# Performance work log

Hardware: AMD Instinct MI355X
Metric: run time of the kernel (lower is better)

## Reference

```python
import jax, jax.numpy as jnp
import numpy as np

V_ENC, V_DEC = 30000, 30000
E_ENC, E_DEC = 256, 256
H = 512
B, S = 64, 48


def gru_cell(x, h, w_ih, w_hh, b_ih, b_hh):
    # torch GRUCell math. x: [B,E], h: [B,H], w_ih: [3H,E], w_hh: [3H,H]
    gi = x @ w_ih.T + b_ih
    gh = h @ w_hh.T + b_hh
    i_r, i_z, i_n = jnp.split(gi, 3, axis=-1)
    h_r, h_z, h_n = jnp.split(gh, 3, axis=-1)
    r = jax.nn.sigmoid(i_r + h_r)
    z = jax.nn.sigmoid(i_z + h_z)
    n = jnp.tanh(i_n + r * h_n)
    return (1.0 - z) * n + z * h


def setup_inputs() -> dict:
    key = jax.random.key(0)
    ks = jax.random.split(key, 14)
    p = lambda k, shp: jax.random.normal(k, shp, dtype=jnp.float32) * 0.05
    return {
        "input_tensor": jax.random.randint(ks[0], (B, S), 0, V_ENC),
        "enc_embed": p(ks[1], (V_ENC, E_ENC)),
        "enc_wih": p(ks[2], (3 * H, E_ENC)),
        "enc_whh": p(ks[3], (3 * H, H)),
        "enc_bih": p(ks[4], (3 * H,)),
        "enc_bhh": p(ks[5], (3 * H,)),
        "dec_embed": p(ks[6], (V_DEC, E_DEC)),
        "dec_wih": p(ks[7], (3 * H, E_DEC)),
        "dec_whh": p(ks[8], (3 * H, H)),
        "dec_bih": p(ks[9], (3 * H,)),
        "dec_bhh": p(ks[10], (3 * H,)),
        "proj_w": p(ks[11], (V_DEC, 2 * H)),
        "proj_b": p(ks[12], (V_DEC,)),
    }


def reference(input_tensor, enc_embed, enc_wih, enc_whh, enc_bih, enc_bhh,
              dec_embed, dec_wih, dec_whh, dec_bih, dec_bhh, proj_w, proj_b):
    batch = input_tensor.shape[0]
    # --- encoder: embedding + GRU over sequence ---
    x_seq = enc_embed[input_tensor]                       # [B,S,E]
    x_seq = jnp.swapaxes(x_seq, 0, 1)                     # [S,B,E]
    h0 = jnp.zeros((batch, H), dtype=enc_embed.dtype)

    def enc_step(h, x):
        h_new = gru_cell(x, h, enc_wih, enc_whh, enc_bih, enc_bhh)
        return h_new, h_new

    enc_last, enc_states = jax.lax.scan(enc_step, h0, x_seq)
    enc_states = jnp.swapaxes(enc_states, 0, 1)           # [B,S,H]

    dec_input0 = jnp.zeros((batch,), dtype=jnp.int32)

    def dec_step(carry, _):
        h, tok = carry
        x = dec_embed[tok]                                # [B,E]
        h_new = gru_cell(x, h, dec_wih, dec_whh, dec_bih, dec_bhh)
        # dot-product attention: decoder hidden vs encoder states
        scores = jnp.einsum("bsh,bh->bs", enc_states, h_new)
        attn = jax.nn.softmax(scores, axis=-1)
        context = jnp.einsum("bs,bsh->bh", attn, enc_states)
        cat = jnp.concatenate([h_new, context], axis=-1)  # [B,2H]
        logits = cat @ proj_w.T + proj_b                  # [B,V]
        log_probs = jax.nn.log_softmax(logits, axis=-1)
        topi = jnp.argmax(log_probs, axis=-1).astype(jnp.int32)
        return (h_new, topi), (topi, log_probs)

    _, (predicted, dists) = jax.lax.scan(
        dec_step, (enc_last, dec_input0), None, length=input_tensor.shape[1])
    return predicted, dists  # [S,B] int, [S,B,V] log-probs
```

## Files before the change

kernel.cpp:

```cpp
#include <hip/hip_runtime.h>
#include <math.h>

#define BB 64
#define SS 48
#define EE 256
#define HH 512
#define VV 30000
#define G3 1536
#define NPB 235
#define TAU 0.04f

typedef __attribute__((ext_vector_type(8))) short s8v;
typedef __attribute__((ext_vector_type(4))) short s4v;
typedef __attribute__((ext_vector_type(4))) float f4v;

__device__ __forceinline__ float sigmoidf_(float x) { return 1.f / (1.f + expf(-x)); }

__device__ __forceinline__ short f2bf(float x) {
    union { float f; unsigned u; } v; v.f = x;
    unsigned r = v.u + 0x7fffu + ((v.u >> 16) & 1u);
    return (short)(r >> 16);
}

__global__ __launch_bounds__(256) void split_hi_kernel(
    const float* __restrict__ src, long n4, short* __restrict__ hi)
{
    for (long i = (long)blockIdx.x * 256 + threadIdx.x; i < n4;
         i += (long)gridDim.x * 256) {
        const float4 x = *(const float4*)&src[i * 4];
        s4v h;
        h[0] = f2bf(x.x); h[1] = f2bf(x.y); h[2] = f2bf(x.z); h[3] = f2bf(x.w);
        *(s4v*)&hi[i * 4] = h;
    }
}

__global__ __launch_bounds__(256) void enc_gi_all_kernel(
    const int* __restrict__ input,
    const float* __restrict__ embed,
    const float* __restrict__ wih,
    float* __restrict__ gi_all)
{
    __shared__ float Wt[64][68];
    __shared__ float Xt[64][68];
    const int t  = threadIdx.x;
    const int tx = t & 15, ty = t >> 4;
    const int j0 = blockIdx.x * 64;
    const int s  = blockIdx.y;
    const int bb = t & 63, kq = t >> 6;
    const int wkk = (t & 15) * 4, wjj = t >> 4;

    const long xrow = (long)input[bb * SS + s] * EE;
    float* gi = gi_all + (long)s * G3 * BB;

    float acc[4][4];
    #pragma unroll
    for (int i = 0; i < 4; i++)
        #pragma unroll
        for (int j = 0; j < 4; j++) acc[i][j] = 0.f;

    for (int kb = 0; kb < EE; kb += 64) {
        #pragma unroll
        for (int r = 0; r < 4; r++) {
            int row = j0 + wjj + r * 16;
            const float4 w = *(const float4*)&wih[row * EE + kb + wkk];
            Wt[wkk + 0][wjj + r * 16] = w.x;
            Wt[wkk + 1][wjj + r * 16] = w.y;
            Wt[wkk + 2][wjj + r * 16] = w.z;
            Wt[wkk + 3][wjj + r * 16] = w.w;
        }
        {
            const float* src = embed + xrow + kb + kq * 16;
            #pragma unroll
            for (int q = 0; q < 4; q++) {
                const float4 x = *(const float4*)&src[q * 4];
                Xt[kq * 16 + q * 4 + 0][bb] = x.x;
                Xt[kq * 16 + q * 4 + 1][bb] = x.y;
                Xt[kq * 16 + q * 4 + 2][bb] = x.z;
                Xt[kq * 16 + q * 4 + 3][bb] = x.w;
            }
        }
        __syncthreads();
        #pragma unroll 8
        for (int k = 0; k < 64; k++) {
            const float4 a = *(const float4*)&Wt[k][ty * 4];
            const float4 x = *(const float4*)&Xt[k][tx * 4];
            acc[0][0] += a.x * x.x; acc[0][1] += a.x * x.y; acc[0][2] += a.x * x.z; acc[0][3] += a.x * x.w;
            acc[1][0] += a.y * x.x; acc[1][1] += a.y * x.y; acc[1][2] += a.y * x.z; acc[1][3] += a.y * x.w;
            acc[2][0] += a.z * x.x; acc[2][1] += a.z * x.y; acc[2][2] += a.z * x.z; acc[2][3] += a.z * x.w;
            acc[3][0] += a.w * x.x; acc[3][1] += a.w * x.y; acc[3][2] += a.w * x.z; acc[3][3] += a.w * x.w;
        }
        __syncthreads();
    }
    #pragma unroll
    for (int i = 0; i < 4; i++) {
        float4 o; o.x = acc[i][0]; o.y = acc[i][1]; o.z = acc[i][2]; o.w = acc[i][3];
        *(float4*)&gi[(j0 + ty * 4 + i) * BB + tx * 4] = o;
    }
}

__global__ __launch_bounds__(256) void enc_step_kernel(
    const float* __restrict__ gi_s,
    const float* __restrict__ whh,
    const float* __restrict__ bih, const float* __restrict__ bhh,
    const float* __restrict__ hprev,
    int s,
    float* __restrict__ enc_states)
{
    __shared__ __attribute__((aligned(16))) float Wt[64][52];
    __shared__ __attribute__((aligned(16))) float Xt[64][68];
    const int t = threadIdx.x;
    const int tx = t & 15, ty = t >> 4;
    const int bb = t & 63, kq = t >> 6;
    const int wlr = t >> 4, wc4 = (t & 15) * 4;
    const int h0 = blockIdx.x * 16;

    float accr[4] = {0.f, 0.f, 0.f, 0.f};
    float accz[4] = {0.f, 0.f, 0.f, 0.f};
    float acchn[4] = {0.f, 0.f, 0.f, 0.f};

    if (hprev) {
        const float* xr = hprev + (long)bb * (SS * HH);
        for (int kb = 0; kb < HH; kb += 64) {
            #pragma unroll
            for (int g = 0; g < 3; g++) {
                const float4 w = *(const float4*)&whh[(long)(g * HH + h0 + wlr) * HH + kb + wc4];
                Wt[wc4 + 0][g * 16 + wlr] = w.x;
                Wt[wc4 + 1][g * 16 + wlr] = w.y;
                Wt[wc4 + 2][g * 16 + wlr] = w.z;
                Wt[wc4 + 3][g * 16 + wlr] = w.w;
            }
            {
                const float* src = xr + kb + kq * 16;
                #pragma unroll
                for (int q = 0; q < 4; q++) {
                    const float4 x = *(const float4*)&src[q * 4];
                    Xt[kq * 16 + q * 4 + 0][bb] = x.x;
                    Xt[kq * 16 + q * 4 + 1][bb] = x.y;
                    Xt[kq * 16 + q * 4 + 2][bb] = x.z;
                    Xt[kq * 16 + q * 4 + 3][bb] = x.w;
                }
            }
            __syncthreads();
            #pragma unroll 4
            for (int k = 0; k < 64; k++) {
                float wr = Wt[k][ty], wz = Wt[k][16 + ty], wn = Wt[k][32 + ty];
                const float4 x = *(const float4*)&Xt[k][tx * 4];
                accr[0] += wr * x.x; accr[1] += wr * x.y; accr[2] += wr * x.z; accr[3] += wr * x.w;
                accz[0] += wz * x.x; accz[1] += wz * x.y; accz[2] += wz * x.z; accz[3] += wz * x.w;
                acchn[0] += wn * x.x; acchn[1] += wn * x.y; acchn[2] += wn * x.z; acchn[3] += wn * x.w;
            }
            __syncthreads();
        }
    }

    const int j = h0 + ty;
    const float br = bih[j] + bhh[j];
    const float bz = bih[HH + j] + bhh[HH + j];
    const float bin = bih[2 * HH + j];
    const float bhn = bhh[2 * HH + j];
    const float4 gr4 = *(const float4*)&gi_s[(long)j * BB + tx * 4];
    const float4 gz4 = *(const float4*)&gi_s[(long)(HH + j) * BB + tx * 4];
    const float4 gn4 = *(const float4*)&gi_s[(long)(2 * HH + j) * BB + tx * 4];
    const float grs[4] = {gr4.x, gr4.y, gr4.z, gr4.w};
    const float gzs[4] = {gz4.x, gz4.y, gz4.z, gz4.w};
    const float gns[4] = {gn4.x, gn4.y, gn4.z, gn4.w};
    #pragma unroll
    for (int i = 0; i < 4; i++) {
        int b = tx * 4 + i;
        float r = sigmoidf_(grs[i] + accr[i] + br);
        float z = sigmoidf_(gzs[i] + accz[i] + bz);
        float n = tanhf(gns[i] + bin + r * (acchn[i] + bhn));
        float hp = hprev ? hprev[(long)b * (SS * HH) + j] : 0.f;
        enc_states[((long)b * SS + s) * HH + j] = (1.f - z) * n + z * hp;
    }
}

__global__ __launch_bounds__(256) void dec_step_kernel(
    const int* __restrict__ tok, int s,
    const float* __restrict__ embed,
    const float* __restrict__ wih, const float* __restrict__ whh,
    const float* __restrict__ bih, const float* __restrict__ bhh,
    const float* __restrict__ hprev, long hstride,
    float* __restrict__ hbuf)
{
    __shared__ __attribute__((aligned(16))) float Wt[64][52];
    __shared__ __attribute__((aligned(16))) float Xt[64][68];
    const int t = threadIdx.x;
    const int tx = t & 15, ty = t >> 4;
    const int bb = t & 63, kq = t >> 6;
    const int wlr = t >> 4, wc4 = (t & 15) * 4;
    const int h0 = blockIdx.x * 16;

    float accr[4] = {0.f, 0.f, 0.f, 0.f};
    float accz[4] = {0.f, 0.f, 0.f, 0.f};
    float accin[4] = {0.f, 0.f, 0.f, 0.f};
    float acchn[4] = {0.f, 0.f, 0.f, 0.f};

    {
        const int tk = (s == 0) ? 0 : tok[bb];
        const float* xr = embed + (long)tk * EE;
        for (int kb = 0; kb < EE; kb += 64) {
            #pragma unroll
            for (int g = 0; g < 3; g++) {
                const float4 w = *(const float4*)&wih[(long)(g * HH + h0 + wlr) * EE + kb + wc4];
                Wt[wc4 + 0][g * 16 + wlr] = w.x;
                Wt[wc4 + 1][g * 16 + wlr] = w.y;
                Wt[wc4 + 2][g * 16 + wlr] = w.z;
                Wt[wc4 + 3][g * 16 + wlr] = w.w;
            }
            {
                const float* src = xr + kb + kq * 16;
                #pragma unroll
                for (int q = 0; q < 4; q++) {
                    const float4 x = *(const float4*)&src[q * 4];
                    Xt[kq * 16 + q * 4 + 0][bb] = x.x;
                    Xt[kq * 16 + q * 4 + 1][bb] = x.y;
                    Xt[kq * 16 + q * 4 + 2][bb] = x.z;
                    Xt[kq * 16 + q * 4 + 3][bb] = x.w;
                }
            }
            __syncthreads();
            #pragma unroll 4
            for (int k = 0; k < 64; k++) {
                float wr = Wt[k][ty], wz = Wt[k][16 + ty], wn = Wt[k][32 + ty];
                const float4 x = *(const float4*)&Xt[k][tx * 4];
                accr[0] += wr * x.x; accr[1] += wr * x.y; accr[2] += wr * x.z; accr[3] += wr * x.w;
                accz[0] += wz * x.x; accz[1] += wz * x.y; accz[2] += wz * x.z; accz[3] += wz * x.w;
                accin[0] += wn * x.x; accin[1] += wn * x.y; accin[2] += wn * x.z; accin[3] += wn * x.w;
            }
            __syncthreads();
        }
    }
    {
        const float* xr = hprev + (long)bb * hstride;
        for (int kb = 0; kb < HH; kb += 64) {
            #pragma unroll
            for (int g = 0; g < 3; g++) {
                const float4 w = *(const float4*)&whh[(long)(g * HH + h0 + wlr) * HH + kb + wc4];
                Wt[wc4 + 0][g * 16 + wlr] = w.x;
                Wt[wc4 + 1][g * 16 + wlr] = w.y;
                Wt[wc4 + 2][g * 16 + wlr] = w.z;
                Wt[wc4 + 3][g * 16 + wlr] = w.w;
            }
            {
                const float* src = xr + kb + kq * 16;
                #pragma unroll
                for (int q = 0; q < 4; q++) {
                    const float4 x = *(const float4*)&src[q * 4];
                    Xt[kq * 16 + q * 4 + 0][bb] = x.x;
                    Xt[kq * 16 + q * 4 + 1][bb] = x.y;
                    Xt[kq * 16 + q * 4 + 2][bb] = x.z;
                    Xt[kq * 16 + q * 4 + 3][bb] = x.w;
                }
            }
            __syncthreads();
            #pragma unroll 4
            for (int k = 0; k < 64; k++) {
                float wr = Wt[k][ty], wz = Wt[k][16 + ty], wn = Wt[k][32 + ty];
                const float4 x = *(const float4*)&Xt[k][tx * 4];
                accr[0] += wr * x.x; accr[1] += wr * x.y; accr[2] += wr * x.z; accr[3] += wr * x.w;
                accz[0] += wz * x.x; accz[1] += wz * x.y; accz[2] += wz * x.z; accz[3] += wz * x.w;
                acchn[0] += wn * x.x; acchn[1] += wn * x.y; acchn[2] += wn * x.z; acchn[3] += wn * x.w;
            }
            __syncthreads();
        }
    }

    const int j = h0 + ty;
    const float br = bih[j] + bhh[j];
    const float bz = bih[HH + j] + bhh[HH + j];
    const float bin = bih[2 * HH + j];
    const float bhn = bhh[2 * HH + j];
    #pragma unroll
    for (int i = 0; i < 4; i++) {
        int b = tx * 4 + i;
        float r = sigmoidf_(accr[i] + br);
        float z = sigmoidf_(accz[i] + bz);
        float n = tanhf(accin[i] + bin + r * (acchn[i] + bhn));
        float hp = hprev[(long)b * hstride + j];
        hbuf[b * HH + j] = (1.f - z) * n + z * hp;
    }
}

__global__ __launch_bounds__(256) void dec_attn_kernel(
    const float* __restrict__ hbuf,
    const float* __restrict__ enc_states,
    float* __restrict__ cat_f32,
    short* __restrict__ cat_hi)
{
    int b = blockIdx.x, t = threadIdx.x;
    __shared__ float hs[HH];
    __shared__ float ctxs[HH];
    __shared__ float sc[SS];

    for (int j = t; j < HH; j += 256) hs[j] = hbuf[b * HH + j];
    __syncthreads();

    int wave = t >> 6, lane = t & 63;
    for (int sp = wave; sp < SS; sp += 4) {
        const float* es = enc_states + ((long)b * SS + sp) * HH;
        float p = 0.f;
        for (int k = lane; k < HH; k += 64) p += es[k] * hs[k];
        for (int o = 32; o; o >>= 1) p += __shfl_down(p, o);
        if (lane == 0) sc[sp] = p;
    }
    __syncthreads();
    if (t == 0) {
        float m = sc[0];
        for (int i = 1; i < SS; i++) m = fmaxf(m, sc[i]);
        float sum = 0.f;
        for (int i = 0; i < SS; i++) { float e = expf(sc[i] - m); sc[i] = e; sum += e; }
        float inv = 1.f / sum;
        for (int i = 0; i < SS; i++) sc[i] *= inv;
    }
    __syncthreads();
    for (int j = t; j < HH; j += 256) {
        float c = 0.f;
        for (int sp = 0; sp < SS; sp++) c += sc[sp] * enc_states[((long)b * SS + sp) * HH + j];
        ctxs[j] = c;
    }
    __syncthreads();
    for (int k = t; k < 2 * HH; k += 256) {
        float val = (k < HH) ? hs[k] : ctxs[k - HH];
        cat_f32[b * 2 * HH + k] = val;
        cat_hi[b * 2 * HH + k] = f2bf(val);
    }
}

__global__ __launch_bounds__(256) void proj_hi_kernel(
    const short* __restrict__ pw_hi,
    const float* __restrict__ pw_f32,
    const short* __restrict__ cat_hi,
    const float* __restrict__ pb,
    float* __restrict__ logits,
    float* __restrict__ pm, float* __restrict__ ps)
{
    __shared__ __attribute__((aligned(16))) char smem_raw[64 * 129 * 4];
    short (*Ah)[72] = (short(*)[72])smem_raw;
    short (*Bh)[72] = (short(*)[72])(smem_raw + 128 * 72 * 2);
    float (*LT)[129] = (float(*)[129])smem_raw;
    __shared__ float sm4[4][64];
    __shared__ float ss4[4][64];

    const int t = threadIdx.x;
    const int lane = t & 63, wave = t >> 6;
    const int v0 = blockIdx.x * 128;

    f4v acc[2][4];
    #pragma unroll
    for (int i = 0; i < 2; i++)
        #pragma unroll
        for (int j = 0; j < 4; j++) acc[i][j] = (f4v){0.f, 0.f, 0.f, 0.f};

    for (int ks = 0; ks < 16; ks++) {
        const int kb = ks * 64;
        if (pw_hi) {
            #pragma unroll
            for (int p = 0; p < 4; p++) {
                int idx = p * 256 + t;
                int r = idx >> 3, c8 = (idx & 7) * 8;
                long vrow = v0 + r; if (vrow >= VV) vrow = VV - 1;
                *(s8v*)&Ah[r][c8] = *(const s8v*)&pw_hi[vrow * 1024 + kb + c8];
            }
        } else {
            #pragma unroll
            for (int p = 0; p < 4; p++) {
                int idx = p * 256 + t;
                int r = idx >> 3, c8 = (idx & 7) * 8;
                long vrow = v0 + r; if (vrow >= VV) vrow = VV - 1;
                const float* src = &pw_f32[vrow * 1024 + kb + c8];
                const float4 f0 = *(const float4*)&src[0];
                const float4 f1 = *(const float4*)&src[4];
                s8v h;
                h[0] = f2bf(f0.x); h[1] = f2bf(f0.y); h[2] = f2bf(f0.z); h[3] = f2bf(f0.w);
                h[4] = f2bf(f1.x); h[5] = f2bf(f1.y); h[6] = f2bf(f1.z); h[7] = f2bf(f1.w);
                *(s8v*)&Ah[r][c8] = h;
            }
        }
        #pragma unroll
        for (int p = 0; p < 2; p++) {
            int idx = p * 256 + t;
            int r = idx >> 3, c8 = (idx & 7) * 8;
            *(s8v*)&Bh[r][c8] = *(const s8v*)&cat_hi[r * 1024 + kb + c8];
        }
        __syncthreads();
        #pragma unroll
        for (int kc = 0; kc < 64; kc += 32) {
            const int ko = kc + (lane >> 4) * 8;
            const int fr = lane & 15;
            s8v ah0 = *(s8v*)&Ah[wave * 32 + fr][ko];
            s8v ah1 = *(s8v*)&Ah[wave * 32 + 16 + fr][ko];
            s8v bh[4];
            #pragma unroll
            for (int fb = 0; fb < 4; fb++) bh[fb] = *(s8v*)&Bh[fb * 16 + fr][ko];
            #pragma unroll
            for (int fb = 0; fb < 4; fb++) {
                acc[0][fb] = __builtin_amdgcn_mfma_f32_16x16x32_bf16(ah0, bh[fb], acc[0][fb], 0, 0, 0);
                acc[1][fb] = __builtin_amdgcn_mfma_f32_16x16x32_bf16(ah1, bh[fb], acc[1][fb], 0, 0, 0);
            }
        }
        __syncthreads();
    }

    const int col = lane & 15;
    #pragma unroll
    for (int fv = 0; fv < 2; fv++) {
        int rloc = wave * 32 + fv * 16 + (lane >> 4) * 4;
        int vbase = v0 + rloc;
        float pbv[4];
        #pragma unroll
        for (int i = 0; i < 4; i++) pbv[i] = (vbase + i < VV) ? pb[vbase + i] : 0.f;
        #pragma unroll
        for (int fb = 0; fb < 4; fb++) {
            int b = fb * 16 + col;
            float o[4];
            #pragma unroll
            for (int i = 0; i < 4; i++) o[i] = acc[fv][fb][i] + pbv[i];
            if (vbase + 3 < VV) {
                float4 st; st.x = o[0]; st.y = o[1]; st.z = o[2]; st.w = o[3];
                *(float4*)&logits[(long)b * VV + vbase] = st;
            } else {
                for (int i = 0; i < 4; i++)
                    if (vbase + i < VV) logits[(long)b * VV + vbase + i] = o[i];
            }
            #pragma unroll
            for (int i = 0; i < 4; i++)
                LT[b][rloc + i] = (vbase + i < VV) ? o[i] : -INFINITY;
        }
    }
    __syncthreads();

    {
        int b = t & 63, q = t >> 6;
        float m = -INFINITY, s = 0.f;
        for (int r = q * 32; r < q * 32 + 32; r++) {
            float v = LT[b][r];
            if (v == -INFINITY) continue;
            if (v > m) { s = s * expf(m - v) + 1.f; m = v; }
            else s += expf(v - m);
        }
        sm4[q][b] = m; ss4[q][b] = s;
    }
    __syncthreads();
    if (t < 64) {
        int b = t;
        float M = sm4[0][b], S = ss4[0][b];
        #pragma unroll
        for (int q = 1; q < 4; q++) {
            float m2 = sm4[q][b], s2 = ss4[q][b];
            if (m2 > M) { S = S * expf(M - m2) + s2; M = m2; }
            else if (m2 != -INFINITY) S += s2 * expf(m2 - M);
        }
        pm[blockIdx.x * 64 + b] = M;
        ps[blockIdx.x * 64 + b] = S;
    }
}

__global__ __launch_bounds__(256) void reduce_par_kernel(
    const float* __restrict__ logits,
    const float* __restrict__ pm, const float* __restrict__ ps,
    const float* __restrict__ pw_f32, const float* __restrict__ pb,
    const float* __restrict__ cat_f32,
    int* __restrict__ tok, float* __restrict__ pred_out, float* __restrict__ lse_out)
{
    int b = blockIdx.x, t = threadIdx.x;
    int lane = t & 63, wave = t >> 6;
    __shared__ float red[256], red2[256];
    __shared__ float cf[2 * HH];
    __shared__ int   qlist[32];
    __shared__ int   vlist[32];
    __shared__ float ws4[4];
    __shared__ float bestv;
    __shared__ int   besti, qcnt, vcnt;

    for (int k = t; k < 2 * HH; k += 256) cf[k] = cat_f32[b * 2 * HH + k];
    if (t == 0) { qcnt = 0; vcnt = 0; bestv = -INFINITY; besti = 0; }

    float pmv = -INFINITY, psv = 0.f;
    if (t < NPB) { pmv = pm[t * 64 + b]; psv = ps[t * 64 + b]; }
    red[t] = pmv; red2[t] = psv;
    __syncthreads();
    for (int o = 128; o; o >>= 1) {
        if (t < o) {
            float m1 = red[t],     s1 = red2[t];
            float m2 = red[t + o], s2 = red2[t + o];
            if (m2 > m1) { red[t] = m2; red2[t] = s2 + s1 * expf(m1 - m2); }
            else if (m2 != -INFINITY) red2[t] = s1 + s2 * expf(m2 - m1);
        }
        __syncthreads();
    }
    float gm  = red[0];
    float lse = gm + logf(red2[0]);
    float thr = gm - TAU;

    if (t < NPB && pmv >= thr) {
        int p = atomicAdd(&qcnt, 1);
        if (p < 32) qlist[p] = t;
    }
    __syncthreads();
    int qn = qcnt; if (qn > 32) qn = 32;

    for (int qi = 0; qi < qn; qi++) {
        int ib = qlist[qi];
        if (t < 128) {
            int v = ib * 128 + t;
            if (v < VV) {
                float lv = logits[(long)b * VV + v];
                if (lv >= thr) {
                    int p = atomicAdd(&vcnt, 1);
                    if (p < 32) vlist[p] = v;
                }
            }
        }
    }
    __syncthreads();
    int nv = vcnt; if (nv > 32) nv = 32;

    for (int c = 0; c < nv; c++) {
        int vr = vlist[c];
        float p = 0.f;
        for (int k = t; k < 2 * HH; k += 256)
            p += pw_f32[(long)vr * 2 * HH + k] * cf[k];
        for (int o = 32; o; o >>= 1) p += __shfl_down(p, o);
        if (lane == 0) ws4[wave] = p;
        __syncthreads();
        if (t == 0) {
            float val = ws4[0] + ws4[1] + ws4[2] + ws4[3] + pb[vr];
            if (val > bestv || (val == bestv && vr < besti)) { bestv = val; besti = vr; }
        }
        __syncthreads();
    }
    if (t == 0) {
        tok[b] = besti;
        pred_out[b] = (float)besti;
        lse_out[b] = lse;
    }
}

__global__ void normalize_kernel(float* __restrict__ dists, const float* __restrict__ stats) {
    const long total4 = (long)SS * BB * VV / 4;
    for (long i4 = (long)blockIdx.x * blockDim.x + threadIdx.x; i4 < total4;
         i4 += (long)gridDim.x * blockDim.x) {
        long i = i4 * 4;
        int sb = (int)(i / VV);
        float st = stats[sb];
        float4 x = *(float4*)&dists[i];
        x.x -= st; x.y -= st; x.z -= st; x.w -= st;
        *(float4*)&dists[i] = x;
    }
}

extern "C" void kernel_launch(void* const* d_in, const int* in_sizes, int n_in,
                              void* d_out, int out_size, void* d_ws, size_t ws_size,
                              hipStream_t stream) {
    const int*   input     = (const int*)  d_in[0];
    const float* enc_embed = (const float*)d_in[1];
    const float* enc_wih   = (const float*)d_in[2];
    const float* enc_whh   = (const float*)d_in[3];
    const float* enc_bih   = (const float*)d_in[4];
    const float* enc_bhh   = (const float*)d_in[5];
    const float* dec_embed = (const float*)d_in[6];
    const float* dec_wih   = (const float*)d_in[7];
    const float* dec_whh   = (const float*)d_in[8];
    const float* dec_bih   = (const float*)d_in[9];
    const float* dec_bhh   = (const float*)d_in[10];
    const float* proj_w    = (const float*)d_in[11];
    const float* proj_b    = (const float*)d_in[12];

    float* out       = (float*)d_out;
    float* pred_out  = out;
    float* dists_out = out + SS * BB;

    float* ws = (float*)d_ws;
    long off = 0;
    float* enc_states = ws + off; off += (long)BB * SS * HH;
    float* gi_all     = ws + off; off += (long)SS * G3 * BB;
    float* hbuf       = ws + off; off += BB * HH;
    float* cat_f32    = ws + off; off += BB * 2 * HH;
    short* cat_hi     = (short*)(ws + off); off += BB * 2 * HH / 2;
    float* pm         = ws + off; off += NPB * 64;
    float* ps         = ws + off; off += NPB * 64;
    float* lse_arr    = ws + off; off += SS * BB;
    int*   tok        = (int*)(ws + off); off += BB;

    const long pw_elems = (long)VV * 2 * HH;
    bool use_split = ((long)ws_size >= (off + pw_elems / 2) * 4 + 1024);
    short* pw_hi = nullptr;
    if (use_split) {
        pw_hi = (short*)(ws + off);
        split_hi_kernel<<<2048, 256, 0, stream>>>(proj_w, pw_elems / 4, pw_hi);
    }

    enc_gi_all_kernel<<<dim3(G3 / 64, SS), 256, 0, stream>>>(input, enc_embed, enc_wih, gi_all);
    for (int s = 0; s < SS; s++) {
        const float* hprev = s ? enc_states + (long)(s - 1) * HH : nullptr;
        enc_step_kernel<<<HH / 16, 256, 0, stream>>>(
            gi_all + (long)s * G3 * BB, enc_whh, enc_bih, enc_bhh,
            hprev, s, enc_states);
    }

    for (int s = 0; s < SS; s++) {
        const float* hprev; long hstride;
        if (s == 0) { hprev = enc_states + (long)(SS - 1) * HH; hstride = (long)SS * HH; }
        else        { hprev = cat_f32;                          hstride = 2 * HH; }

        dec_step_kernel<<<HH / 16, 256, 0, stream>>>(tok, s, dec_embed,
                                                     dec_wih, dec_whh, dec_bih, dec_bhh,
                                                     hprev, hstride, hbuf);
        dec_attn_kernel<<<BB, 256, 0, stream>>>(hbuf, enc_states, cat_f32, cat_hi);
        float* logits = dists_out + (long)s * BB * VV;
        proj_hi_kernel<<<NPB, 256, 0, stream>>>(pw_hi, proj_w, cat_hi, proj_b, logits, pm, ps);
        reduce_par_kernel<<<BB, 256, 0, stream>>>(logits, pm, ps, proj_w, proj_b, cat_f32,
                                                  tok, pred_out + s * BB, lse_arr + s * BB);
    }

    normalize_kernel<<<2048, 256, 0, stream>>>(dists_out, lse_arr);
}
```

Measured before the change: 6.169 ms.

## Persist encoder recurrence in one kernel and fuse decoder GRU, attention, argmax

```diff
diff --git a/kernel.cpp b/kernel.cpp
--- a/kernel.cpp
+++ b/kernel.cpp
@@ -20,6 +20,9 @@
     union { float f; unsigned u; } v; v.f = x;
     unsigned r = v.u + 0x7fffu + ((v.u >> 16) & 1u);
     return (short)(r >> 16);
+}
+__device__ __forceinline__ float dot4_(float4 a, float4 b) {
+    return a.x * b.x + a.y * b.y + a.z * b.z + a.w * b.w;
 }
 
 __global__ __launch_bounds__(256) void split_hi_kernel(
@@ -98,205 +101,195 @@
     }
 }
 
-__global__ __launch_bounds__(256) void enc_step_kernel(
-    const float* __restrict__ gi_s,
+__global__ __launch_bounds__(256) void enc_all_kernel(
+    const float* __restrict__ gi_all,
     const float* __restrict__ whh,
     const float* __restrict__ bih, const float* __restrict__ bhh,
-    const float* __restrict__ hprev,
-    int s,
     float* __restrict__ enc_states)
 {
-    __shared__ __attribute__((aligned(16))) float Wt[64][52];
-    __shared__ __attribute__((aligned(16))) float Xt[64][68];
-    const int t = threadIdx.x;
-    const int tx = t & 15, ty = t >> 4;
-    const int bb = t & 63, kq = t >> 6;
-    const int wlr = t >> 4, wc4 = (t & 15) * 4;
-    const int h0 = blockIdx.x * 16;
-
-    float accr[4] = {0.f, 0.f, 0.f, 0.f};
-    float accz[4] = {0.f, 0.f, 0.f, 0.f};
-    float acchn[4] = {0.f, 0.f, 0.f, 0.f};
-
-    if (hprev) {
-        const float* xr = hprev + (long)bb * (SS * HH);
-        for (int kb = 0; kb < HH; kb += 64) {
-            #pragma unroll
-            for (int g = 0; g < 3; g++) {
-                const float4 w = *(const float4*)&whh[(long)(g * HH + h0 + wlr) * HH + kb + wc4];
-                Wt[wc4 + 0][g * 16 + wlr] = w.x;
-                Wt[wc4 + 1][g * 16 + wlr] = w.y;
-                Wt[wc4 + 2][g * 16 + wlr] = w.z;
-                Wt[wc4 + 3][g * 16 + wlr] = w.w;
-            }
-            {
-                const float* src = xr + kb + kq * 16;
-                #pragma unroll
-                for (int q = 0; q < 4; q++) {
-                    const float4 x = *(const float4*)&src[q * 4];
-                    Xt[kq * 16 + q * 4 + 0][bb] = x.x;
-                    Xt[kq * 16 + q * 4 + 1][bb] = x.y;
-                    Xt[kq * 16 + q * 4 + 2][bb] = x.z;
-                    Xt[kq * 16 + q * 4 + 3][bb] = x.w;
-                }
-            }
-            __syncthreads();
-            #pragma unroll 4
-            for (int k = 0; k < 64; k++) {
-                float wr = Wt[k][ty], wz = Wt[k][16 + ty], wn = Wt[k][32 + ty];
-                const float4 x = *(const float4*)&Xt[k][tx * 4];
-                accr[0] += wr * x.x; accr[1] += wr * x.y; accr[2] += wr * x.z; accr[3] += wr * x.w;
-                accz[0] += wz * x.x; accz[1] += wz * x.y; accz[2] += wz * x.z; accz[3] += wz * x.w;
-                acchn[0] += wn * x.x; acchn[1] += wn * x.y; acchn[2] += wn * x.z; acchn[3] += wn * x.w;
-            }
-            __syncthreads();
-        }
-    }
-
-    const int j = h0 + ty;
-    const float br = bih[j] + bhh[j];
-    const float bz = bih[HH + j] + bhh[HH + j];
-    const float bin = bih[2 * HH + j];
-    const float bhn = bhh[2 * HH + j];
-    const float4 gr4 = *(const float4*)&gi_s[(long)j * BB + tx * 4];
-    const float4 gz4 = *(const float4*)&gi_s[(long)(HH + j) * BB + tx * 4];
-    const float4 gn4 = *(const float4*)&gi_s[(long)(2 * HH + j) * BB + tx * 4];
-    const float grs[4] = {gr4.x, gr4.y, gr4.z, gr4.w};
-    const float gzs[4] = {gz4.x, gz4.y, gz4.z, gz4.w};
-    const float gns[4] = {gn4.x, gn4.y, gn4.z, gn4.w};
-    #pragma unroll
-    for (int i = 0; i < 4; i++) {
-        int b = tx * 4 + i;
-        float r = sigmoidf_(grs[i] + accr[i] + br);
-        float z = sigmoidf_(gzs[i] + accz[i] + bz);
-        float n = tanhf(gns[i] + bin + r * (acchn[i] + bhn));
-        float hp = hprev ? hprev[(long)b * (SS * HH) + j] : 0.f;
-        enc_states[((long)b * SS + s) * HH + j] = (1.f - z) * n + z * hp;
-    }
-}
-
-__global__ __launch_bounds__(256) void dec_step_kernel(
-    const int* __restrict__ tok, int s,
+    const int b = blockIdx.x, t = threadIdx.x;
+    const int lane = t & 63, wave = t >> 6;
+    __shared__ float hp[2][HH];
+
+    for (int j = t; j < HH; j += 256) {
+        float gr = gi_all[(long)j * BB + b];
+        float gz = gi_all[(long)(HH + j) * BB + b];
+        float gn = gi_all[(long)(2 * HH + j) * BB + b];
+        float r = sigmoidf_(gr + bih[j] + bhh[j]);
+        float z = sigmoidf_(gz + bih[HH + j] + bhh[HH + j]);
+        float n = tanhf(gn + bih[2 * HH + j] + r * bhh[2 * HH + j]);
+        float h = (1.f - z) * n;
+        hp[0][j] = h;
+        enc_states[((long)b * SS) * HH + j] = h;
+    }
+    __syncthreads();
+
+    for (int s = 1; s < SS; s++) {
+        const int cur = (s - 1) & 1, nxt = s & 1;
+        const float* gis = gi_all + (long)s * G3 * BB;
+        const float4 x0 = *(const float4*)&hp[cur][lane * 8];
+        const float4 x1 = *(const float4*)&hp[cur][lane * 8 + 4];
+        for (int i = 0; i < 128; i++) {
+            const int j = wave * 128 + i;
+            const float* wr = whh + (long)j * HH + lane * 8;
+            const float* wz = whh + (long)(HH + j) * HH + lane * 8;
+            const float* wn = whh + (long)(2 * HH + j) * HH + lane * 8;
+            float pr = dot4_(*(const float4*)&wr[0], x0) + dot4_(*(const float4*)&wr[4], x1);
+            float pz = dot4_(*(const float4*)&wz[0], x0) + dot4_(*(const float4*)&wz[4], x1);
+            float pn = dot4_(*(const float4*)&wn[0], x0) + dot4_(*(const float4*)&wn[4], x1);
+            #pragma unroll
+            for (int o = 32; o; o >>= 1) {
+                pr += __shfl_down(pr, o);
+                pz += __shfl_down(pz, o);
+                pn += __shfl_down(pn, o);
+            }
+            if (lane == 0) {
+                float gr = gis[(long)j * BB + b];
+                float gz = gis[(long)(HH + j) * BB + b];
+                float gn = gis[(long)(2 * HH + j) * BB + b];
+                float r = sigmoidf_(gr + pr + bih[j] + bhh[j]);
+                float z = sigmoidf_(gz + pz + bih[HH + j] + bhh[HH + j]);
+                float n = tanhf(gn + bih[2 * HH + j] + r * (pn + bhh[2 * HH + j]));
+                float h = (1.f - z) * n + z * hp[cur][j];
+                hp[nxt][j] = h;
+                enc_states[((long)b * SS + s) * HH + j] = h;
+            }
+        }
+        __syncthreads();
+    }
+}
+
+__global__ __launch_bounds__(256) void dec_fused_kernel(
+    int s,
+    const float* __restrict__ pm, const float* __restrict__ ps,
+    const float* __restrict__ logits_prev,
+    const float* __restrict__ pw_f32, const float* __restrict__ pb,
+    float* __restrict__ pred_out, float* __restrict__ lse_arr,
     const float* __restrict__ embed,
     const float* __restrict__ wih, const float* __restrict__ whh,
     const float* __restrict__ bih, const float* __restrict__ bhh,
-    const float* __restrict__ hprev, long hstride,
-    float* __restrict__ hbuf)
+    const float* __restrict__ enc_states,
+    float* __restrict__ cat_f32, short* __restrict__ cat_hi)
 {
-    __shared__ __attribute__((aligned(16))) float Wt[64][52];
-    __shared__ __attribute__((aligned(16))) float Xt[64][68];
-    const int t = threadIdx.x;
-    const int tx = t & 15, ty = t >> 4;
-    const int bb = t & 63, kq = t >> 6;
-    const int wlr = t >> 4, wc4 = (t & 15) * 4;
-    const int h0 = blockIdx.x * 16;
-
-    float accr[4] = {0.f, 0.f, 0.f, 0.f};
-    float accz[4] = {0.f, 0.f, 0.f, 0.f};
-    float accin[4] = {0.f, 0.f, 0.f, 0.f};
-    float acchn[4] = {0.f, 0.f, 0.f, 0.f};
+    const int b = blockIdx.x, t = threadIdx.x;
+    const int lane = t & 63, wave = t >> 6;
+    __shared__ float cf[2 * HH];
+    __shared__ float xe[EE];
+    __shared__ float hs[HH], ctxs[HH], sc[SS];
+    __shared__ float red[256], red2[256];
+    __shared__ int qlist[32], vlist[32];
+    __shared__ float ws4[4];
+    __shared__ float bestv;
+    __shared__ int besti, qcnt, vcnt;
+
+    int tk = 0;
+
+    if (s > 0) {
+        for (int k = t; k < 2 * HH; k += 256) cf[k] = cat_f32[(long)b * 2 * HH + k];
+        if (t == 0) { qcnt = 0; vcnt = 0; bestv = -INFINITY; besti = 0; }
+
+        float pmv = -INFINITY, psv = 0.f;
+        if (t < NPB) { pmv = pm[t * 64 + b]; psv = ps[t * 64 + b]; }
+        red[t] = pmv; red2[t] = psv;
+        __syncthreads();
+        for (int o = 128; o; o >>= 1) {
+            if (t < o) {
+                float m1 = red[t],     s1 = red2[t];
+                float m2 = red[t + o], s2 = red2[t + o];
+                if (m2 > m1) { red[t] = m2; red2[t] = s2 + s1 * expf(m1 - m2); }
+                else if (m2 != -INFINITY) red2[t] = s1 + s2 * expf(m2 - m1);
+            }
+            __syncthreads();
+        }
+        float gm  = red[0];
+        float lse = gm + logf(red2[0]);
+        float thr = gm - TAU;
+
+        if (t < NPB && pmv >= thr) {
+            int p = atomicAdd(&qcnt, 1);
+            if (p < 32) qlist[p] = t;
+        }
+        __syncthreads();
+        int qn = qcnt; if (qn > 32) qn = 32;
+        for (int qi = 0; qi < qn; qi++) {
+            int ib = qlist[qi];
+            if (t < 128) {
+                int v = ib * 128 + t;
+                if (v < VV) {
+                    float lv = logits_prev[(long)b * VV + v];
+                    if (lv >= thr) {
+                        int p = atomicAdd(&vcnt, 1);
+                        if (p < 32) vlist[p] = v;
+                    }
+                }
+            }
+        }
+        __syncthreads();
+        int nv = vcnt; if (nv > 32) nv = 32;
+        for (int c = 0; c < nv; c++) {
+            int vr = vlist[c];
+            float p = 0.f;
+            for (int k = t; k < 2 * HH; k += 256)
+                p += pw_f32[(long)vr * 2 * HH + k] * cf[k];
+            for (int o = 32; o; o >>= 1) p += __shfl_down(p, o);
+            if (lane == 0) ws4[wave] = p;
+            __syncthreads();
+            if (t == 0) {
+                float val = ws4[0] + ws4[1] + ws4[2] + ws4[3] + pb[vr];
+                if (val > bestv || (val == bestv && vr < besti)) { bestv = val; besti = vr; }
+            }
+            __syncthreads();
+        }
+        if (t == 0) {
+            pred_out[(s - 1) * BB + b] = (float)besti;
+            lse_arr[(s - 1) * BB + b] = lse;
+        }
+        __syncthreads();
+        tk = besti;
+    } else {
+        for (int j = t; j < HH; j += 256)
+            cf[j] = enc_states[((long)b * SS + (SS - 1)) * HH + j];
+        __syncthreads();
+    }
+
+    for (int k = t; k < EE; k += 256) xe[k] = embed[(long)tk * EE + k];
+    __syncthreads();
 
     {
-        const int tk = (s == 0) ? 0 : tok[bb];
-        const float* xr = embed + (long)tk * EE;
-        for (int kb = 0; kb < EE; kb += 64) {
-            #pragma unroll
-            for (int g = 0; g < 3; g++) {
-                const float4 w = *(const float4*)&wih[(long)(g * HH + h0 + wlr) * EE + kb + wc4];
-                Wt[wc4 + 0][g * 16 + wlr] = w.x;
-                Wt[wc4 + 1][g * 16 + wlr] = w.y;
-                Wt[wc4 + 2][g * 16 + wlr] = w.z;
-                Wt[wc4 + 3][g * 16 + wlr] = w.w;
-            }
-            {
-                const float* src = xr + kb + kq * 16;
-                #pragma unroll
-                for (int q = 0; q < 4; q++) {
-                    const float4 x = *(const float4*)&src[q * 4];
-                    Xt[kq * 16 + q * 4 + 0][bb] = x.x;
-                    Xt[kq * 16 + q * 4 + 1][bb] = x.y;
-                    Xt[kq * 16 + q * 4 + 2][bb] = x.z;
-                    Xt[kq * 16 + q * 4 + 3][bb] = x.w;
-                }
-            }
-            __syncthreads();
-            #pragma unroll 4
-            for (int k = 0; k < 64; k++) {
-                float wr = Wt[k][ty], wz = Wt[k][16 + ty], wn = Wt[k][32 + ty];
-                const float4 x = *(const float4*)&Xt[k][tx * 4];
-                accr[0] += wr * x.x; accr[1] += wr * x.y; accr[2] += wr * x.z; accr[3] += wr * x.w;
-                accz[0] += wz * x.x; accz[1] += wz * x.y; accz[2] += wz * x.z; accz[3] += wz * x.w;
-                accin[0] += wn * x.x; accin[1] += wn * x.y; accin[2] += wn * x.z; accin[3] += wn * x.w;
-            }
-            __syncthreads();
-        }
-    }
-    {
-        const float* xr = hprev + (long)bb * hstride;
-        for (int kb = 0; kb < HH; kb += 64) {
-            #pragma unroll
-            for (int g = 0; g < 3; g++) {
-                const float4 w = *(const float4*)&whh[(long)(g * HH + h0 + wlr) * HH + kb + wc4];
-                Wt[wc4 + 0][g * 16 + wlr] = w.x;
-                Wt[wc4 + 1][g * 16 + wlr] = w.y;
-                Wt[wc4 + 2][g * 16 + wlr] = w.z;
-                Wt[wc4 + 3][g * 16 + wlr] = w.w;
-            }
-            {
-                const float* src = xr + kb + kq * 16;
-                #pragma unroll
-                for (int q = 0; q < 4; q++) {
-                    const float4 x = *(const float4*)&src[q * 4];
-                    Xt[kq * 16 + q * 4 + 0][bb] = x.x;
-                    Xt[kq * 16 + q * 4 + 1][bb] = x.y;
-                    Xt[kq * 16 + q * 4 + 2][bb] = x.z;
-                    Xt[kq * 16 + q * 4 + 3][bb] = x.w;
-                }
-            }
-            __syncthreads();
-            #pragma unroll 4
-            for (int k = 0; k < 64; k++) {
-                float wr = Wt[k][ty], wz = Wt[k][16 + ty], wn = Wt[k][32 + ty];
-                const float4 x = *(const float4*)&Xt[k][tx * 4];
-                accr[0] += wr * x.x; accr[1] += wr * x.y; accr[2] += wr * x.z; accr[3] += wr * x.w;
-                accz[0] += wz * x.x; accz[1] += wz * x.y; accz[2] += wz * x.z; accz[3] += wz * x.w;
-                acchn[0] += wn * x.x; acchn[1] += wn * x.y; acchn[2] += wn * x.z; acchn[3] += wn * x.w;
-            }
-            __syncthreads();
-        }
-    }
-
-    const int j = h0 + ty;
-    const float br = bih[j] + bhh[j];
-    const float bz = bih[HH + j] + bhh[HH + j];
-    const float bin = bih[2 * HH + j];
-    const float bhn = bhh[2 * HH + j];
-    #pragma unroll
-    for (int i = 0; i < 4; i++) {
-        int b = tx * 4 + i;
-        float r = sigmoidf_(accr[i] + br);
-        float z = sigmoidf_(accz[i] + bz);
-        float n = tanhf(accin[i] + bin + r * (acchn[i] + bhn));
-        float hp = hprev[(long)b * hstride + j];
-        hbuf[b * HH + j] = (1.f - z) * n + z * hp;
-    }
-}
-
-__global__ __launch_bounds__(256) void dec_attn_kernel(
-    const float* __restrict__ hbuf,
-    const float* __restrict__ enc_states,
-    float* __restrict__ cat_f32,
-    short* __restrict__ cat_hi)
-{
-    int b = blockIdx.x, t = threadIdx.x;
-    __shared__ float hs[HH];
-    __shared__ float ctxs[HH];
-    __shared__ float sc[SS];
-
-    for (int j = t; j < HH; j += 256) hs[j] = hbuf[b * HH + j];
-    __syncthreads();
-
-    int wave = t >> 6, lane = t & 63;
+        const float4 xi  = *(const float4*)&xe[lane * 4];
+        const float4 h0  = *(const float4*)&cf[lane * 8];
+        const float4 h1  = *(const float4*)&cf[lane * 8 + 4];
+        for (int i = 0; i < 128; i++) {
+            const int j = wave * 128 + i;
+            const float* ar = wih + (long)j * EE + lane * 4;
+            const float* az = wih + (long)(HH + j) * EE + lane * 4;
+            const float* an = wih + (long)(2 * HH + j) * EE + lane * 4;
+            float pr   = dot4_(*(const float4*)ar, xi);
+            float pz   = dot4_(*(const float4*)az, xi);
+            float pnih = dot4_(*(const float4*)an, xi);
+            const float* vr = whh + (long)j * HH + lane * 8;
+            const float* vz = whh + (long)(HH + j) * HH + lane * 8;
+            const float* vn = whh + (long)(2 * HH + j) * HH + lane * 8;
+            pr += dot4_(*(const float4*)&vr[0], h0) + dot4_(*(const float4*)&vr[4], h1);
+            pz += dot4_(*(const float4*)&vz[0], h0) + dot4_(*(const float4*)&vz[4], h1);
+            float pnhh = dot4_(*(const float4*)&vn[0], h0) + dot4_(*(const float4*)&vn[4], h1);
+            #pragma unroll
+            for (int o = 32; o; o >>= 1) {
+                pr   += __shfl_down(pr, o);
+                pz   += __shfl_down(pz, o);
+                pnih += __shfl_down(pnih, o);
+                pnhh += __shfl_down(pnhh, o);
+            }
+            if (lane == 0) {
+                float r = sigmoidf_(pr + bih[j] + bhh[j]);
+                float z = sigmoidf_(pz + bih[HH + j] + bhh[HH + j]);
+                float n = tanhf(pnih + bih[2 * HH + j] + r * (pnhh + bhh[2 * HH + j]));
+                hs[j] = (1.f - z) * n + z * cf[j];
+            }
+        }
+    }
+    __syncthreads();
+
     for (int sp = wave; sp < SS; sp += 4) {
         const float* es = enc_states + ((long)b * SS + sp) * HH;
         float p = 0.f;
@@ -316,14 +309,15 @@
     __syncthreads();
     for (int j = t; j < HH; j += 256) {
         float c = 0.f;
-        for (int sp = 0; sp < SS; sp++) c += sc[sp] * enc_states[((long)b * SS + sp) * HH + j];
+        for (int sp = 0; sp < SS; sp++)
+            c += sc[sp] * enc_states[((long)b * SS + sp) * HH + j];
         ctxs[j] = c;
     }
     __syncthreads();
     for (int k = t; k < 2 * HH; k += 256) {
         float val = (k < HH) ? hs[k] : ctxs[k - HH];
-        cat_f32[b * 2 * HH + k] = val;
-        cat_hi[b * 2 * HH + k] = f2bf(val);
+        cat_f32[(long)b * 2 * HH + k] = val;
+        cat_hi[(long)b * 2 * HH + k] = f2bf(val);
     }
 }
 
@@ -575,7 +569,6 @@
     long off = 0;
     float* enc_states = ws + off; off += (long)BB * SS * HH;
     float* gi_all     = ws + off; off += (long)SS * G3 * BB;
-    float* hbuf       = ws + off; off += BB * HH;
     float* cat_f32    = ws + off; off += BB * 2 * HH;
     short* cat_hi     = (short*)(ws + off); off += BB * 2 * HH / 2;
     float* pm         = ws + off; off += NPB * 64;
@@ -592,27 +585,21 @@
     }
 
     enc_gi_all_kernel<<<dim3(G3 / 64, SS), 256, 0, stream>>>(input, enc_embed, enc_wih, gi_all);
+    enc_all_kernel<<<BB, 256, 0, stream>>>(gi_all, enc_whh, enc_bih, enc_bhh, enc_states);
+
     for (int s = 0; s < SS; s++) {
-        const float* hprev = s ? enc_states + (long)(s - 1) * HH : nullptr;
-        enc_step_kernel<<<HH / 16, 256, 0, stream>>>(
-            gi_all + (long)s * G3 * BB, enc_whh, enc_bih, enc_bhh,
-            hprev, s, enc_states);
-    }
-
-    for (int s = 0; s < SS; s++) {
-        const float* hprev; long hstride;
-        if (s == 0) { hprev = enc_states + (long)(SS - 1) * HH; hstride = (long)SS * HH; }
-        else        { hprev = cat_f32;                          hstride = 2 * HH; }
-
-        dec_step_kernel<<<HH / 16, 256, 0, stream>>>(tok, s, dec_embed,
-                                                     dec_wih, dec_whh, dec_bih, dec_bhh,
-                                                     hprev, hstride, hbuf);
-        dec_attn_kernel<<<BB, 256, 0, stream>>>(hbuf, enc_states, cat_f32, cat_hi);
+        const float* logits_prev = (s > 0) ? (dists_out + (long)(s - 1) * BB * VV) : dists_out;
+        dec_fused_kernel<<<BB, 256, 0, stream>>>(
+            s, pm, ps, logits_prev, proj_w, proj_b,
+            pred_out, lse_arr,
+            dec_embed, dec_wih, dec_whh, dec_bih, dec_bhh,
+            enc_states, cat_f32, cat_hi);
         float* logits = dists_out + (long)s * BB * VV;
         proj_hi_kernel<<<NPB, 256, 0, stream>>>(pw_hi, proj_w, cat_hi, proj_b, logits, pm, ps);
-        reduce_par_kernel<<<BB, 256, 0, stream>>>(logits, pm, ps, proj_w, proj_b, cat_f32,
-                                                  tok, pred_out + s * BB, lse_arr + s * BB);
-    }
+    }
+    reduce_par_kernel<<<BB, 256, 0, stream>>>(
+        dists_out + (long)(SS - 1) * BB * VV, pm, ps, proj_w, proj_b, cat_f32,
+        tok, pred_out + (SS - 1) * BB, lse_arr + (SS - 1) * BB);
 
     normalize_kernel<<<2048, 256, 0, stream>>>(dists_out, lse_arr);
 }
```

After: 16.38 ms. +165.6%, slower.

## Persistent encoder kernel with grid flags; fold normalization into next projection

Applied to the files above, without the earlier changes.

```diff
diff --git a/kernel.cpp b/kernel.cpp
--- a/kernel.cpp
+++ b/kernel.cpp
@@ -9,6 +9,7 @@
 #define G3 1536
 #define NPB 235
 #define TAU 0.04f
+#define NENC 48
 
 typedef __attribute__((ext_vector_type(8))) short s8v;
 typedef __attribute__((ext_vector_type(4))) short s4v;
@@ -20,6 +21,20 @@
     union { float f; unsigned u; } v; v.f = x;
     unsigned r = v.u + 0x7fffu + ((v.u >> 16) & 1u);
     return (short)(r >> 16);
+}
+
+__device__ __forceinline__ void frel(unsigned* f) {
+    __syncthreads();
+    __threadfence();
+    if (threadIdx.x == 0) atomicAdd(f, 1u);
+}
+__device__ __forceinline__ void fwait(unsigned* f, unsigned target) {
+    if (threadIdx.x == 0) {
+        while (__hip_atomic_load(f, __ATOMIC_RELAXED, __HIP_MEMORY_SCOPE_AGENT) < target)
+            __builtin_amdgcn_s_sleep(2);
+    }
+    __syncthreads();
+    __threadfence();
 }
 
 __global__ __launch_bounds__(256) void split_hi_kernel(
@@ -98,80 +113,104 @@
     }
 }
 
-__global__ __launch_bounds__(256) void enc_step_kernel(
-    const float* __restrict__ gi_s,
-    const float* __restrict__ whh,
-    const float* __restrict__ bih, const float* __restrict__ bhh,
-    const float* __restrict__ hprev,
-    int s,
-    float* __restrict__ enc_states)
-{
-    __shared__ __attribute__((aligned(16))) float Wt[64][52];
-    __shared__ __attribute__((aligned(16))) float Xt[64][68];
-    const int t = threadIdx.x;
+__device__ __forceinline__ void gemm32x64(
+    const float* __restrict__ W, int K, int j0,
+    const float* __restrict__ embed, const int* __restrict__ tokv, int s,
+    const float* __restrict__ xbase, long xstride,
+    float* __restrict__ outp,
+    float (*Wt)[34], float (*Xt)[68])
+{
+    const int t  = threadIdx.x;
     const int tx = t & 15, ty = t >> 4;
     const int bb = t & 63, kq = t >> 6;
-    const int wlr = t >> 4, wc4 = (t & 15) * 4;
-    const int h0 = blockIdx.x * 16;
-
-    float accr[4] = {0.f, 0.f, 0.f, 0.f};
-    float accz[4] = {0.f, 0.f, 0.f, 0.f};
-    float acchn[4] = {0.f, 0.f, 0.f, 0.f};
-
-    if (hprev) {
-        const float* xr = hprev + (long)bb * (SS * HH);
-        for (int kb = 0; kb < HH; kb += 64) {
-            #pragma unroll
-            for (int g = 0; g < 3; g++) {
-                const float4 w = *(const float4*)&whh[(long)(g * HH + h0 + wlr) * HH + kb + wc4];
-                Wt[wc4 + 0][g * 16 + wlr] = w.x;
-                Wt[wc4 + 1][g * 16 + wlr] = w.y;
-                Wt[wc4 + 2][g * 16 + wlr] = w.z;
-                Wt[wc4 + 3][g * 16 + wlr] = w.w;
-            }
-            {
-                const float* src = xr + kb + kq * 16;
-                #pragma unroll
-                for (int q = 0; q < 4; q++) {
-                    const float4 x = *(const float4*)&src[q * 4];
-                    Xt[kq * 16 + q * 4 + 0][bb] = x.x;
-                    Xt[kq * 16 + q * 4 + 1][bb] = x.y;
-                    Xt[kq * 16 + q * 4 + 2][bb] = x.z;
-                    Xt[kq * 16 + q * 4 + 3][bb] = x.w;
-                }
-            }
-            __syncthreads();
-            #pragma unroll 4
-            for (int k = 0; k < 64; k++) {
-                float wr = Wt[k][ty], wz = Wt[k][16 + ty], wn = Wt[k][32 + ty];
-                const float4 x = *(const float4*)&Xt[k][tx * 4];
-                accr[0] += wr * x.x; accr[1] += wr * x.y; accr[2] += wr * x.z; accr[3] += wr * x.w;
-                accz[0] += wz * x.x; accz[1] += wz * x.y; accz[2] += wz * x.z; accz[3] += wz * x.w;
-                acchn[0] += wn * x.x; acchn[1] += wn * x.y; acchn[2] += wn * x.z; acchn[3] += wn * x.w;
-            }
-            __syncthreads();
-        }
-    }
-
-    const int j = h0 + ty;
-    const float br = bih[j] + bhh[j];
-    const float bz = bih[HH + j] + bhh[HH + j];
-    const float bin = bih[2 * HH + j];
-    const float bhn = bhh[2 * HH + j];
-    const float4 gr4 = *(const float4*)&gi_s[(long)j * BB + tx * 4];
-    const float4 gz4 = *(const float4*)&gi_s[(long)(HH + j) * BB + tx * 4];
-    const float4 gn4 = *(const float4*)&gi_s[(long)(2 * HH + j) * BB + tx * 4];
-    const float grs[4] = {gr4.x, gr4.y, gr4.z, gr4.w};
-    const float gzs[4] = {gz4.x, gz4.y, gz4.z, gz4.w};
-    const float gns[4] = {gn4.x, gn4.y, gn4.z, gn4.w};
-    #pragma unroll
-    for (int i = 0; i < 4; i++) {
-        int b = tx * 4 + i;
-        float r = sigmoidf_(grs[i] + accr[i] + br);
-        float z = sigmoidf_(gzs[i] + accz[i] + bz);
-        float n = tanhf(gns[i] + bin + r * (acchn[i] + bhn));
-        float hp = hprev ? hprev[(long)b * (SS * HH) + j] : 0.f;
-        enc_states[((long)b * SS + s) * HH + j] = (1.f - z) * n + z * hp;
+    const int jr = t >> 3, kc = (t & 7) * 8;
+
+    const float* xr;
+    if (embed) { int tk = (s == 0) ? 0 : tokv[bb]; xr = embed + (long)tk * EE; }
+    else       { xr = xbase + (long)bb * xstride; }
+
+    float acc0[4] = {0.f, 0.f, 0.f, 0.f};
+    float acc1[4] = {0.f, 0.f, 0.f, 0.f};
+
+    for (int kb = 0; kb < K; kb += 64) {
+        {
+            const float* wsrc = &W[(long)(j0 + jr) * K + kb + kc];
+            const float4 w0 = *(const float4*)&wsrc[0];
+            const float4 w1 = *(const float4*)&wsrc[4];
+            Wt[kc + 0][jr] = w0.x; Wt[kc + 1][jr] = w0.y;
+            Wt[kc + 2][jr] = w0.z; Wt[kc + 3][jr] = w0.w;
+            Wt[kc + 4][jr] = w1.x; Wt[kc + 5][jr] = w1.y;
+            Wt[kc + 6][jr] = w1.z; Wt[kc + 7][jr] = w1.w;
+        }
+        {
+            const float* src = xr + kb + kq * 16;
+            #pragma unroll
+            for (int q = 0; q < 4; q++) {
+                const float4 x = *(const float4*)&src[q * 4];
+                Xt[kq * 16 + q * 4 + 0][bb] = x.x;
+                Xt[kq * 16 + q * 4 + 1][bb] = x.y;
+                Xt[kq * 16 + q * 4 + 2][bb] = x.z;
+                Xt[kq * 16 + q * 4 + 3][bb] = x.w;
+            }
+        }
+        __syncthreads();
+        #pragma unroll 4
+        for (int k = 0; k < 64; k++) {
+            const float2 w = *(const float2*)&Wt[k][ty * 2];
+            const float4 x = *(const float4*)&Xt[k][tx * 4];
+            acc0[0] += w.x * x.x; acc0[1] += w.x * x.y; acc0[2] += w.x * x.z; acc0[3] += w.x * x.w;
+            acc1[0] += w.y * x.x; acc1[1] += w.y * x.y; acc1[2] += w.y * x.z; acc1[3] += w.y * x.w;
+        }
+        __syncthreads();
+    }
+    float4 o0; o0.x = acc0[0]; o0.y = acc0[1]; o0.z = acc0[2]; o0.w = acc0[3];
+    float4 o1; o1.x = acc1[0]; o1.y = acc1[1]; o1.z = acc1[2]; o1.w = acc1[3];
+    *(float4*)&outp[(long)(j0 + ty * 2 + 0) * BB + tx * 4] = o0;
+    *(float4*)&outp[(long)(j0 + ty * 2 + 1) * BB + tx * 4] = o1;
+}
+
+__global__ __launch_bounds__(256) void enc_persist_kernel(
+    const float* __restrict__ gi_all, const float* __restrict__ whh,
+    const float* __restrict__ bih, const float* __restrict__ bhh,
+    float* __restrict__ enc_states, float* __restrict__ gh,
+    unsigned* __restrict__ flg)
+{
+    __shared__ __attribute__((aligned(16))) float Wt[64][34];
+    __shared__ __attribute__((aligned(16))) float Xt[64][68];
+    const int bid = blockIdx.x, t = threadIdx.x;
+    const int j0 = bid * 32;
+    unsigned* eG = flg;
+    unsigned* eC = flg + 48;
+
+    for (int s = 0; s < SS; s++) {
+        if (s == 0) {
+            float4* dst = (float4*)&gh[(long)j0 * BB];
+            for (int i = t; i < 32 * BB / 4; i += 256) dst[i] = (float4){0.f, 0.f, 0.f, 0.f};
+        } else {
+            fwait(&eC[s - 1], NENC);
+            gemm32x64(whh, HH, j0, nullptr, nullptr, s,
+                      enc_states + (long)(s - 1) * HH, (long)SS * HH, gh, Wt, Xt);
+        }
+        frel(&eG[s]);
+        fwait(&eG[s], NENC);
+        {
+            const float* gi = gi_all + (long)s * G3 * BB;
+            for (int idx = bid * 256 + t; idx < BB * HH; idx += NENC * 256) {
+                int b = idx & 63, j = idx >> 6;
+                float ir  = gi[j * BB + b]            + bih[j];
+                float iz  = gi[(HH + j) * BB + b]     + bih[HH + j];
+                float in_ = gi[(2 * HH + j) * BB + b] + bih[2 * HH + j];
+                float hr  = gh[j * BB + b]            + bhh[j];
+                float hz  = gh[(HH + j) * BB + b]     + bhh[HH + j];
+                float hn  = gh[(2 * HH + j) * BB + b] + bhh[2 * HH + j];
+                float r = sigmoidf_(ir + hr);
+                float z = sigmoidf_(iz + hz);
+                float n = tanhf(in_ + r * hn);
+                float hp = s ? enc_states[((long)b * SS + (s - 1)) * HH + j] : 0.f;
+                enc_states[((long)b * SS + s) * HH + j] = (1.f - z) * n + z * hp;
+            }
+        }
+        frel(&eC[s]);
     }
 }
 
@@ -333,7 +372,9 @@
     const short* __restrict__ cat_hi,
     const float* __restrict__ pb,
     float* __restrict__ logits,
-    float* __restrict__ pm, float* __restrict__ ps)
+    float* __restrict__ pm, float* __restrict__ ps,
+    float* __restrict__ prev_logits,
+    const float* __restrict__ lse_prev)
 {
     __shared__ __attribute__((aligned(16))) char smem_raw[64 * 129 * 4];
     short (*Ah)[72] = (short(*)[72])smem_raw;
@@ -454,6 +495,17 @@
         pm[blockIdx.x * 64 + b] = M;
         ps[blockIdx.x * 64 + b] = S;
     }
+
+    if (prev_logits) {
+        const long total4 = (long)BB * VV / 4;
+        for (long i4 = (long)blockIdx.x * 256 + t; i4 < total4; i4 += (long)NPB * 256) {
+            long i = i4 * 4;
+            float l = lse_prev[(int)(i / VV)];
+            float4 x = *(float4*)&prev_logits[i];
+            x.x -= l; x.y -= l; x.z -= l; x.w -= l;
+            *(float4*)&prev_logits[i] = x;
+        }
+    }
 }
 
 __global__ __launch_bounds__(256) void reduce_par_kernel(
@@ -537,16 +589,17 @@
     }
 }
 
-__global__ void normalize_kernel(float* __restrict__ dists, const float* __restrict__ stats) {
-    const long total4 = (long)SS * BB * VV / 4;
-    for (long i4 = (long)blockIdx.x * blockDim.x + threadIdx.x; i4 < total4;
-         i4 += (long)gridDim.x * blockDim.x) {
+__global__ __launch_bounds__(256) void norm_last_kernel(
+    float* __restrict__ prev_logits, const float* __restrict__ lse_prev)
+{
+    const long total4 = (long)BB * VV / 4;
+    for (long i4 = (long)blockIdx.x * 256 + threadIdx.x; i4 < total4;
+         i4 += (long)gridDim.x * 256) {
         long i = i4 * 4;
-        int sb = (int)(i / VV);
-        float st = stats[sb];
-        float4 x = *(float4*)&dists[i];
-        x.x -= st; x.y -= st; x.z -= st; x.w -= st;
-        *(float4*)&dists[i] = x;
+        float l = lse_prev[(int)(i / VV)];
+        float4 x = *(float4*)&prev_logits[i];
+        x.x -= l; x.y -= l; x.z -= l; x.w -= l;
+        *(float4*)&prev_logits[i] = x;
     }
 }
 
@@ -573,15 +626,17 @@
 
     float* ws = (float*)d_ws;
     long off = 0;
-    float* enc_states = ws + off; off += (long)BB * SS * HH;
-    float* gi_all     = ws + off; off += (long)SS * G3 * BB;
-    float* hbuf       = ws + off; off += BB * HH;
-    float* cat_f32    = ws + off; off += BB * 2 * HH;
-    short* cat_hi     = (short*)(ws + off); off += BB * 2 * HH / 2;
-    float* pm         = ws + off; off += NPB * 64;
-    float* ps         = ws + off; off += NPB * 64;
-    float* lse_arr    = ws + off; off += SS * BB;
-    int*   tok        = (int*)(ws + off); off += BB;
+    float*    enc_states = ws + off; off += (long)BB * SS * HH;
+    float*    gi_all     = ws + off; off += (long)SS * G3 * BB;
+    float*    gh_enc     = ws + off; off += G3 * BB;
+    float*    hbuf       = ws + off; off += BB * HH;
+    float*    cat_f32    = ws + off; off += BB * 2 * HH;
+    short*    cat_hi     = (short*)(ws + off); off += BB * 2 * HH / 2;
+    float*    pm         = ws + off; off += NPB * 64;
+    float*    ps         = ws + off; off += NPB * 64;
+    float*    lse_arr    = ws + off; off += SS * BB;
+    int*      tok        = (int*)(ws + off); off += BB;
+    unsigned* flg        = (unsigned*)(ws + off); off += 1024;
 
     const long pw_elems = (long)VV * 2 * HH;
     bool use_split = ((long)ws_size >= (off + pw_elems / 2) * 4 + 1024);
@@ -591,13 +646,10 @@
         split_hi_kernel<<<2048, 256, 0, stream>>>(proj_w, pw_elems / 4, pw_hi);
     }
 
+    hipMemsetAsync(flg, 0, 1024 * sizeof(unsigned), stream);
     enc_gi_all_kernel<<<dim3(G3 / 64, SS), 256, 0, stream>>>(input, enc_embed, enc_wih, gi_all);
-    for (int s = 0; s < SS; s++) {
-        const float* hprev = s ? enc_states + (long)(s - 1) * HH : nullptr;
-        enc_step_kernel<<<HH / 16, 256, 0, stream>>>(
-            gi_all + (long)s * G3 * BB, enc_whh, enc_bih, enc_bhh,
-            hprev, s, enc_states);
-    }
+    enc_persist_kernel<<<NENC, 256, 0, stream>>>(gi_all, enc_whh, enc_bih, enc_bhh,
+                                                 enc_states, gh_enc, flg);
 
     for (int s = 0; s < SS; s++) {
         const float* hprev; long hstride;
@@ -608,11 +660,16 @@
                                                      dec_wih, dec_whh, dec_bih, dec_bhh,
                                                      hprev, hstride, hbuf);
         dec_attn_kernel<<<BB, 256, 0, stream>>>(hbuf, enc_states, cat_f32, cat_hi);
+
         float* logits = dists_out + (long)s * BB * VV;
-        proj_hi_kernel<<<NPB, 256, 0, stream>>>(pw_hi, proj_w, cat_hi, proj_b, logits, pm, ps);
+        float* prev_logits = (s > 0) ? (dists_out + (long)(s - 1) * BB * VV) : nullptr;
+        const float* lse_prev = (s > 0) ? (lse_arr + (s - 1) * BB) : nullptr;
+        proj_hi_kernel<<<NPB, 256, 0, stream>>>(pw_hi, proj_w, cat_hi, proj_b, logits, pm, ps,
+                                                prev_logits, lse_prev);
         reduce_par_kernel<<<BB, 256, 0, stream>>>(logits, pm, ps, proj_w, proj_b, cat_f32,
                                                   tok, pred_out + s * BB, lse_arr + s * BB);
     }
 
-    normalize_kernel<<<2048, 256, 0, stream>>>(dists_out, lse_arr);
-}
+    norm_last_kernel<<<512, 256, 0, stream>>>(dists_out + (long)(SS - 1) * BB * VV,
+                                              lse_arr + (SS - 1) * BB);
+}
```

Measured after the change: 6.692 ms. 8.5% more time.
